# Kernel optimization log

Hardware: AMD Instinct MI355X
Metric: run time of the kernel (lower is better)

The kernel has to match this reference:

```python
import jax, jax.numpy as jnp
import numpy as np

D_MODEL = 1024
NHEAD = 16
EPS = 1e-5


def layer_norm(x, scale, bias):
    mu = jnp.mean(x, axis=-1, keepdims=True)
    var = jnp.var(x, axis=-1, keepdims=True)
    return (x - mu) * jax.lax.rsqrt(var + EPS) * scale + bias


def setup_inputs() -> dict:
    key = jax.random.key(0)
    ks = jax.random.split(key, 8)
    B, S, D = 4, 2048, D_MODEL
    s = 1.0 / np.sqrt(D)
    return {
        "x": jax.random.normal(ks[0], (B, S, D), dtype=jnp.float32),
        "Wq": jax.random.normal(ks[1], (D, D), dtype=jnp.float32) * s,
        "Wk": jax.random.normal(ks[2], (D, D), dtype=jnp.float32) * s,
        "Wv": jax.random.normal(ks[3], (D, D), dtype=jnp.float32) * s,
        "W1": jax.random.normal(ks[4], (D, D), dtype=jnp.float32) * s,
        "b1": jnp.zeros((D,), dtype=jnp.float32),
        "W2": jax.random.normal(ks[5], (D, D), dtype=jnp.float32) * s,
        "b2": jnp.zeros((D,), dtype=jnp.float32),
        "ln1_scale": jnp.ones((D,), dtype=jnp.float32),
        "ln1_bias": jnp.zeros((D,), dtype=jnp.float32),
        "ln2_scale": jnp.ones((D,), dtype=jnp.float32),
        "ln2_bias": jnp.zeros((D,), dtype=jnp.float32),
    }


def reference(x, Wq, Wk, Wv, W1, b1, W2, b2, ln1_scale, ln1_bias, ln2_scale, ln2_bias):
    B, S, D = x.shape
    H = NHEAD
    dh = D // H
    x = layer_norm(x, ln1_scale, ln1_bias)
    # torch Linear: y = x @ W.T (no bias for q/k/v)
    q = jnp.einsum('bsd,ed->bse', x, Wq).reshape(B, S, H, dh).transpose(0, 2, 1, 3)
    k = jnp.einsum('bsd,ed->bse', x, Wk).reshape(B, S, H, dh).transpose(0, 2, 1, 3)
    v = jnp.einsum('bsd,ed->bse', x, Wv).reshape(B, S, H, dh).transpose(0, 2, 1, 3)
    # NOTE: original module applies NO 1/sqrt(dh) scaling — kept faithful.
    scores = jnp.einsum('bhqd,bhkd->bhqk', q, k)
    attn = jax.nn.softmax(scores, axis=-1)  # dropout is identity in eval
    att = jnp.einsum('bhqk,bhkd->bhqd', attn, v)
    att = att.transpose(0, 2, 1, 3).reshape(B, S, D)
    xt = layer_norm(x + att, ln2_scale, ln2_bias)
    h = jax.nn.relu(jnp.einsum('bsd,ed->bse', xt, W1) + b1)
    ffn = jnp.einsum('bsd,ed->bse', h, W2) + b2
    return xt + ffn
```

## Files before the change

kernel.cpp:

```cpp
#include <hip/hip_runtime.h>
#include <stdint.h>

typedef unsigned short u16;
typedef __attribute__((ext_vector_type(4))) float f32x4;
typedef _Float16 h16;
typedef __attribute__((ext_vector_type(8))) _Float16 f16x8;
typedef __attribute__((ext_vector_type(4))) _Float16 h16x4;
typedef __attribute__((ext_vector_type(2))) __fp16 fp16v2;

#define DMODEL 1024
#define SEQ    2048
#define BATCH  4
#define NHEAD  16
#define DH     64
#define NTOK   (BATCH*SEQ)
#define BH     (BATCH*NHEAD)
#define EPS    1e-5f
#define LOG2E  1.44269504f

__device__ __forceinline__ void gload_lds16(const void* g, void* l){
  __builtin_amdgcn_global_load_lds((__attribute__((address_space(1))) unsigned int*)g,
                                   (__attribute__((address_space(3))) unsigned int*)l,
                                   16, 0, 0);
}

__device__ __forceinline__ float fastexp2(float x){
#if __has_builtin(__builtin_amdgcn_exp2f)
  return __builtin_amdgcn_exp2f(x);
#else
  return exp2f(x);
#endif
}

__device__ __forceinline__ int swzkey(int row){ return (row&7) ^ ((row>>3)&7); }

__global__ __launch_bounds__(256) void prep_weights(const float* __restrict__ Wq,
                                                    const float* __restrict__ Wk,
                                                    const float* __restrict__ Wv,
                                                    const float* __restrict__ W1,
                                                    const float* __restrict__ W2,
                                                    h16* __restrict__ wqkv,
                                                    h16* __restrict__ w1h,
                                                    h16* __restrict__ w2h){
  const int nW = DMODEL*DMODEL;
  int r = blockIdx.x >> 10;
  int i = ((blockIdx.x & 1023)*256 + threadIdx.x)*4;
  const float* src = (r==0) ? Wq : (r==1) ? Wk : (r==2) ? Wv : (r==3) ? W1 : W2;
  h16* dst = (r==0) ? wqkv : (r==1) ? (wqkv+nW) : (r==2) ? (wqkv+2*nW) : (r==3) ? w1h : w2h;
  float4 v = *reinterpret_cast<const float4*>(src + i);
  h16x4 o; o[0]=(h16)v.x; o[1]=(h16)v.y; o[2]=(h16)v.z; o[3]=(h16)v.w;
  *reinterpret_cast<h16x4*>(dst + i) = o;
}

__global__ __launch_bounds__(256) void ln_kernel(const float* __restrict__ in0,
                                                 const float* __restrict__ sc,
                                                 const float* __restrict__ bi,
                                                 float* __restrict__ of32,
                                                 h16* __restrict__ oh16){
  int row = blockIdx.x*4 + (threadIdx.x>>6);
  int l = threadIdx.x & 63;
  size_t rbase = (size_t)row*DMODEL;
  float v[16];
  #pragma unroll
  for (int q=0;q<4;++q){
    float4 t = *reinterpret_cast<const float4*>(in0 + rbase + q*256 + l*4);
    v[q*4]=t.x; v[q*4+1]=t.y; v[q*4+2]=t.z; v[q*4+3]=t.w;
  }
  float s=0.f, ss=0.f;
  #pragma unroll
  for (int j=0;j<16;++j){ s += v[j]; ss += v[j]*v[j]; }
  #pragma unroll
  for (int m=1;m<64;m<<=1){ s += __shfl_xor(s,m); ss += __shfl_xor(ss,m); }
  float mu  = s * (1.0f/DMODEL);
  float var = fmaxf(ss * (1.0f/DMODEL) - mu*mu, 0.0f);
  float r = rsqrtf(var + EPS);
  #pragma unroll
  for (int q=0;q<4;++q){
    float4 g = *reinterpret_cast<const float4*>(sc + q*256 + l*4);
    float4 b = *reinterpret_cast<const float4*>(bi + q*256 + l*4);
    float o0 = (v[q*4  ]-mu)*r*g.x + b.x;
    float o1 = (v[q*4+1]-mu)*r*g.y + b.y;
    float o2 = (v[q*4+2]-mu)*r*g.z + b.z;
    float o3 = (v[q*4+3]-mu)*r*g.w + b.w;
    size_t off = rbase + q*256 + l*4;
    if (of32){
      float4 ov; ov.x=o0; ov.y=o1; ov.z=o2; ov.w=o3;
      *reinterpret_cast<float4*>(of32 + off) = ov;
    }
    if (oh16){
      h16x4 oh; oh[0]=(h16)o0; oh[1]=(h16)o1; oh[2]=(h16)o2; oh[3]=(h16)o3;
      *reinterpret_cast<h16x4*>(oh16 + off) = oh;
    }
  }
}

__global__ __launch_bounds__(256) void gemm_qkv(const h16* __restrict__ xn,
                                                const h16* __restrict__ wqkv,
                                                h16* __restrict__ qT,
                                                h16* __restrict__ kR,
                                                h16* __restrict__ vT){
  const int K = DMODEL;
  __shared__ h16 As[2][128*64], Bs[2][128*64];
  int id = blockIdx.x;
  int xcd = id & 7, j = id >> 3;
  int bm = xcd*8 + j/24;
  int bn = j - (j/24)*24;
  int t = threadIdx.x, l = t&63, w = t>>6;
  int wr = w>>1, wc = w&1;
  const h16* Bsrc = wqkv + (size_t)bn*128*K;

  f32x4 acc[4][4];
  #pragma unroll
  for (int m=0;m<4;++m)
    #pragma unroll
    for (int n=0;n<4;++n)
      #pragma unroll
      for (int i=0;i<4;++i) acc[m][n][i] = 0.0f;

  #define QSTAGE(bb, k0)                                                          \
    { _Pragma("unroll")                                                           \
      for (int i_=0;i_<4;++i_){                                                   \
        int slot = i_*256 + t;                                                    \
        int row = slot>>3, pc = slot&7;                                           \
        int lc = pc ^ swzkey(row);                                                \
        gload_lds16(xn + (size_t)(bm*128 + row)*K + (k0) + lc*8, &As[bb][slot*8]);\
        gload_lds16(Bsrc + (size_t)row*K + (k0) + lc*8, &Bs[bb][slot*8]);         \
      } }

  const int nk = K/64;
  QSTAGE(0, 0);
  int cur = 0;
  for (int kt=0; kt<nk; ++kt){
    __syncthreads();
    if (kt+1 < nk) QSTAGE(cur^1, (kt+1)*64);
    #pragma unroll
    for (int ks=0; ks<2; ++ks){
      f16x8 af[4], bf[4];
      #pragma unroll
      for (int m=0;m<4;++m){
        int row = wr*64 + m*16 + (l&15);
        int cp = (ks*4 + (l>>4)) ^ swzkey(row);
        af[m] = *reinterpret_cast<const f16x8*>(&As[cur][row*64 + cp*8]);
      }
      #pragma unroll
      for (int n=0;n<4;++n){
        int row = wc*64 + n*16 + (l&15);
        int cp = (ks*4 + (l>>4)) ^ swzkey(row);
        bf[n] = *reinterpret_cast<const f16x8*>(&Bs[cur][row*64 + cp*8]);
      }
      __builtin_amdgcn_s_setprio(1);
      #pragma unroll
      for (int m=0;m<4;++m)
        #pragma unroll
        for (int n=0;n<4;++n)
          acc[m][n] = __builtin_amdgcn_mfma_f32_16x16x32_f16(af[m], bf[n], acc[m][n], 0,0,0);
      __builtin_amdgcn_s_setprio(0);
    }
    cur ^= 1;
  }

  const bool isK = (bn >= 8 && bn < 16);
  const bool isQ = (bn < 8);
  #pragma unroll
  for (int m=0;m<4;++m){
    int row0 = bm*128 + wr*64 + m*16 + ((l>>4)<<2);
    int b = row0 >> 11, s0 = row0 & 2047;
    #pragma unroll
    for (int n=0;n<4;++n){
      int col = bn*128 + wc*64 + n*16 + (l&15);
      int dg = col & 1023;
      int hh = dg >> 6, dh = dg & 63;
      if (isK){
        #pragma unroll
        for (int i=0;i<4;++i)
          kR[((size_t)(b*NHEAD + hh)*SEQ + s0 + i)*DH + dh] = (h16)acc[m][n][i];
      } else {
        h16x4 ov;
        #pragma unroll
        for (int i=0;i<4;++i){
          float vv = acc[m][n][i];
          if (isQ) vv *= LOG2E;
          ov[i] = (h16)vv;
        }
        int s0p = isQ ? s0 : ((s0 & ~31) + (((s0>>2)&3)<<3) + (((s0>>4)&1)<<2));
        h16* dst = (isQ ? qT : vT) + ((size_t)(b*NHEAD + hh)*DH + dh)*SEQ + s0p;
        *reinterpret_cast<h16x4*>(dst) = ov;
      }
    }
  }
}

template<bool RELU, bool RES, bool OUTF32>
__global__ __launch_bounds__(256) void gemm_ffn(const h16* __restrict__ A,
                                                const h16* __restrict__ W,
                                                const float* __restrict__ bias,
                                                const float* __restrict__ resid,
                                                void* __restrict__ outp,
                                                int M, int N, int K){
  __shared__ h16 As[2][128*64];
  __shared__ h16 Bs[2][128*64];
  int id = blockIdx.x;
  int xcd = id & 7, j = id >> 3;
  int nbn = N >> 7;
  int bm = xcd*((M>>7)>>3) + j/nbn;
  int bn = j - (j/nbn)*nbn;
  int t = threadIdx.x, l = t&63, w = t>>6;
  int wr = w>>1, wc = w&1;
  f32x4 acc[4][4];
  #pragma unroll
  for (int m=0;m<4;++m)
    #pragma unroll
    for (int n=0;n<4;++n)
      #pragma unroll
      for (int i=0;i<4;++i) acc[m][n][i] = 0.0f;

  #define FSTAGE(bb, k0)                                                          \
    { _Pragma("unroll")                                                           \
      for (int i_=0;i_<4;++i_){                                                   \
        int slot = i_*256 + t;                                                    \
        int row = slot>>3, pc = slot&7;                                           \
        int lc = pc ^ swzkey(row);                                                \
        gload_lds16(A + (size_t)(bm*128 + row)*K + (k0) + lc*8, &As[bb][slot*8]); \
        gload_lds16(W + (size_t)(bn*128 + row)*K + (k0) + lc*8, &Bs[bb][slot*8]); \
      } }

  const int nk = K/64;
  FSTAGE(0, 0);
  int cur = 0;
  for (int kt=0; kt<nk; ++kt){
    __syncthreads();
    if (kt+1 < nk) FSTAGE(cur^1, (kt+1)*64);
    #pragma unroll
    for (int ks=0; ks<2; ++ks){
      f16x8 af[4], bf[4];
      #pragma unroll
      for (int m=0;m<4;++m){
        int row = wr*64 + m*16 + (l&15);
        int cp = (ks*4 + (l>>4)) ^ swzkey(row);
        af[m] = *reinterpret_cast<const f16x8*>(&As[cur][row*64 + cp*8]);
      }
      #pragma unroll
      for (int n=0;n<4;++n){
        int row = wc*64 + n*16 + (l&15);
        int cp = (ks*4 + (l>>4)) ^ swzkey(row);
        bf[n] = *reinterpret_cast<const f16x8*>(&Bs[cur][row*64 + cp*8]);
      }
      __builtin_amdgcn_s_setprio(1);
      #pragma unroll
      for (int m=0;m<4;++m)
        #pragma unroll
        for (int n=0;n<4;++n)
          acc[m][n] = __builtin_amdgcn_mfma_f32_16x16x32_f16(af[m], bf[n], acc[m][n], 0,0,0);
      __builtin_amdgcn_s_setprio(0);
    }
    cur ^= 1;
  }

  #pragma unroll
  for (int m=0;m<4;++m){
    int row0 = bm*128 + wr*64 + m*16 + ((l>>4)<<2);
    #pragma unroll
    for (int n=0;n<4;++n){
      int col = bn*128 + wc*64 + n*16 + (l&15);
      float bv = bias[col];
      #pragma unroll
      for (int i=0;i<4;++i){
        float vv = acc[m][n][i] + bv;
        if (RELU) vv = fmaxf(vv, 0.0f);
        size_t off = (size_t)(row0+i)*N + col;
        if (RES) vv += resid[off];
        if (OUTF32) ((float*)outp)[off] = vv;
        else        ((h16*)outp)[off] = (h16)vv;
      }
    }
  }
}

#define QBLK 256
#define KBLK 64
#define RESC_THR_L2 11.5415603f
#define NROWS (BH*8*256)

__global__ __launch_bounds__(512, 2) void attn_split(const h16* __restrict__ qT,
                                                     const h16* __restrict__ kR,
                                                     const h16* __restrict__ vT,
                                                     h16* __restrict__ outP0,
                                                     h16* __restrict__ outP1,
                                                     float2* __restrict__ lm){
  int id = blockIdx.x;
  int bh   = (id & 7) + ((id >> 7) << 3);
  int qb   = (id >> 3) & 7;
  int half = (id >> 6) & 1;
  int t = threadIdx.x, l = t&63, w = t>>6;
  int g = l>>4;

  const size_t hbase = (size_t)bh * SEQ * DH;
  const h16* khb = kR + hbase + (size_t)half*(SEQ/2)*DH;
  const h16* qtb = qT + hbase;
  const h16* vtb = vT + hbase + half*(SEQ/2);
  int q0 = qb*QBLK + w*32;

  f16x8 qf[2][2];
  #pragma unroll
  for (int qs=0;qs<2;++qs)
    #pragma unroll
    for (int kc=0;kc<2;++kc)
      #pragma unroll
      for (int j=0;j<8;++j)
        qf[qs][kc][j] = qtb[(size_t)(kc*32 + g*8 + j)*SEQ + q0 + qs*16 + (l&15)];

  __shared__ h16 Kh2[2][KBLK*64];
  __shared__ h16 Vt2[2][KBLK*64];

  int offs[8];
  #pragma unroll
  for (int kc=0;kc<2;++kc)
    #pragma unroll
    for (int st=0;st<4;++st){
      int rr = st*16 + (l&15);
      offs[kc*4+st] = rr*128 + (((kc*4 + g) ^ swzkey(rr))<<4);
    }

  int srow = t>>3, spc = t&7;
  int slc = spc ^ swzkey(srow);
  const h16* ksrc = khb + (size_t)srow*DH + slc*8;
  const h16* vsrc = vtb + (size_t)srow*SEQ + slc*8;

  f32x4 o[2][4];
  #pragma unroll
  for (int qs=0;qs<2;++qs)
    #pragma unroll
    for (int dt=0;dt<4;++dt)
      #pragma unroll
      for (int i=0;i<4;++i) o[qs][dt][i] = 0.0f;
  f32x4 lacc[2];
  #pragma unroll
  for (int qs=0;qs<2;++qs)
    #pragma unroll
    for (int i=0;i<4;++i) lacc[qs][i] = 0.0f;
  float m_run[2] = {-3.0e38f, -3.0e38f};

  f16x8 onesA;
  #pragma unroll
  for (int j=0;j<8;++j) onesA[j] = (h16)1.0f;

  #define STAGE(bb)                                  \
    { gload_lds16(ksrc, &Kh2[bb][t*8]);              \
      gload_lds16(vsrc, &Vt2[bb][t*8]);              \
      ksrc += KBLK*DH; vsrc += KBLK; }

  STAGE(0);
  int cur = 0;
  const int NT = SEQ/2/KBLK;
  for (int kt=0; kt<NT; ++kt){
    __syncthreads();
    if (kt+1 < NT) STAGE(cur^1);

    char* KhB = (char*)&Kh2[cur][0];
    char* VtB = (char*)&Vt2[cur][0];

    f32x4 sc[2][4];
    #pragma unroll
    for (int qs=0;qs<2;++qs)
      #pragma unroll
      for (int st=0;st<4;++st)
        #pragma unroll
        for (int i=0;i<4;++i) sc[qs][st][i] = 0.0f;

    #pragma unroll
    for (int kc=0;kc<2;++kc)
      #pragma unroll
      for (int st=0;st<4;++st){
        f16x8 kf = *reinterpret_cast<const f16x8*>(KhB + offs[kc*4+st]);
        __builtin_amdgcn_s_setprio(1);
        sc[0][st] = __builtin_amdgcn_mfma_f32_16x16x32_f16(kf, qf[0][kc], sc[0][st], 0,0,0);
        sc[1][st] = __builtin_amdgcn_mfma_f32_16x16x32_f16(kf, qf[1][kc], sc[1][st], 0,0,0);
        __builtin_amdgcn_s_setprio(0);
      }

    float lmax[2];
    #pragma unroll
    for (int qs=0;qs<2;++qs){
      const float* s = (const float*)&sc[qs][0];
      float m0 = fmaxf(s[0], s[1]);
      #pragma unroll
      for (int j=2;j<16;j+=2) m0 = fmaxf(fmaxf(m0, s[j]), s[j+1]);
      lmax[qs] = m0;
    }
    bool defer = (__all((lmax[0] <= m_run[0] + RESC_THR_L2) &&
                        (lmax[1] <= m_run[1] + RESC_THR_L2)) != 0);
    if (!defer){
      #pragma unroll
      for (int qs=0;qs<2;++qs){
        float m0 = lmax[qs];
        m0 = fmaxf(m0, __shfl_xor(m0, 16));
        m0 = fmaxf(m0, __shfl_xor(m0, 32));
        float mn = fmaxf(m_run[qs], m0);
        float scl = fastexp2(m_run[qs] - mn);
        m_run[qs] = mn;
        #pragma unroll
        for (int dt=0;dt<4;++dt)
          #pragma unroll
          for (int i=0;i<4;++i) o[qs][dt][i] *= scl;
        #pragma unroll
        for (int i=0;i<4;++i) lacc[qs][i] *= scl;
      }
    }

    union { unsigned u[4]; f16x8 v; } pfu[2][2];
    #pragma unroll
    for (int qs=0;qs<2;++qs){
      float mn = m_run[qs];
      const float* s = (const float*)&sc[qs][0];
      #pragma unroll
      for (int kc=0;kc<2;++kc)
        #pragma unroll
        for (int j=0;j<4;++j){
          float p0 = fastexp2(s[kc*8+2*j]   - mn);
          float p1 = fastexp2(s[kc*8+2*j+1] - mn);
          union { fp16v2 v2; unsigned u; } c;
          c.v2 = __builtin_amdgcn_cvt_pkrtz(p0, p1);
          pfu[qs][kc].u[j] = c.u;
        }
    }

    #pragma unroll
    for (int kc=0;kc<2;++kc){
      __builtin_amdgcn_s_setprio(1);
      lacc[0] = __builtin_amdgcn_mfma_f32_16x16x32_f16(onesA, pfu[0][kc].v, lacc[0], 0,0,0);
      lacc[1] = __builtin_amdgcn_mfma_f32_16x16x32_f16(onesA, pfu[1][kc].v, lacc[1], 0,0,0);
      __builtin_amdgcn_s_setprio(0);
      #pragma unroll
      for (int dt=0;dt<4;++dt){
        f16x8 vf = *reinterpret_cast<const f16x8*>(VtB + offs[kc*4+dt]);
        __builtin_amdgcn_s_setprio(1);
        o[0][dt] = __builtin_amdgcn_mfma_f32_16x16x32_f16(vf, pfu[0][kc].v, o[0][dt], 0,0,0);
        o[1][dt] = __builtin_amdgcn_mfma_f32_16x16x32_f16(vf, pfu[1][kc].v, o[1][dt], 0,0,0);
        __builtin_amdgcn_s_setprio(0);
      }
    }
    cur ^= 1;
  }

  h16* outP = half ? outP1 : outP0;
  int rowbase = (bh*8 + qb)*256 + w*32;
  #pragma unroll
  for (int qs=0;qs<2;++qs){
    float lt = lacc[qs][0];
    float inv = 1.0f / lt;
    int row = rowbase + qs*16 + (l&15);
    #pragma unroll
    for (int dt=0;dt<4;++dt){
      h16x4 ov;
      #pragma unroll
      for (int i=0;i<4;++i) ov[i] = (h16)(o[qs][dt][i] * inv);
      *reinterpret_cast<h16x4*>(outP + (size_t)row*64 + dt*16 + (g<<2)) = ov;
    }
    if (l < 16)
      lm[half*NROWS + row] = make_float2(m_run[qs], lt);
  }
}

__global__ __launch_bounds__(256) void ln2_combine(const float* __restrict__ xn,
                                                   const h16* __restrict__ p0,
                                                   const h16* __restrict__ p1,
                                                   const float2* __restrict__ lm,
                                                   const float* __restrict__ sc,
                                                   const float* __restrict__ bi,
                                                   float* __restrict__ of32,
                                                   h16* __restrict__ oh16){
  int token = blockIdx.x*4 + (threadIdx.x>>6);
  int l = threadIdx.x & 63;
  int b = token >> 11, qb = (token >> 8) & 7, r = token & 255;
  int hh = l >> 2;
  int rowg = ((b*NHEAD + hh)*8 + qb)*256 + r;
  float2 A = lm[rowg];
  float2 B = lm[NROWS + rowg];
  float ms = fmaxf(A.x, B.x);
  float w0 = A.y * fastexp2(A.x - ms);
  float w1 = B.y * fastexp2(B.x - ms);
  float inv = 1.0f / (w0 + w1);
  w0 *= inv; w1 *= inv;

  const f16x8* q0 = reinterpret_cast<const f16x8*>(p0 + (size_t)rowg*64 + (l&3)*16);
  const f16x8* q1 = reinterpret_cast<const f16x8*>(p1 + (size_t)rowg*64 + (l&3)*16);
  size_t base = (size_t)token*DMODEL + l*16;
  float v[16];
  #pragma unroll
  for (int c=0;c<2;++c){
    f16x8 a = q0[c], bb = q1[c];
    #pragma unroll
    for (int j=0;j<8;++j)
      v[c*8+j] = (float)a[j]*w0 + (float)bb[j]*w1;
  }
  #pragma unroll
  for (int q=0;q<4;++q){
    float4 t = *reinterpret_cast<const float4*>(xn + base + q*4);
    v[q*4] += t.x; v[q*4+1] += t.y; v[q*4+2] += t.z; v[q*4+3] += t.w;
  }

  float s=0.f, ss=0.f;
  #pragma unroll
  for (int j=0;j<16;++j){ s += v[j]; ss += v[j]*v[j]; }
  #pragma unroll
  for (int m=1;m<64;m<<=1){ s += __shfl_xor(s,m); ss += __shfl_xor(ss,m); }
  float mu  = s * (1.0f/DMODEL);
  float var = fmaxf(ss * (1.0f/DMODEL) - mu*mu, 0.0f);
  float rr = rsqrtf(var + EPS);
  #pragma unroll
  for (int q=0;q<4;++q){
    float4 g = *reinterpret_cast<const float4*>(sc + l*16 + q*4);
    float4 bb = *reinterpret_cast<const float4*>(bi + l*16 + q*4);
    float o0 = (v[q*4  ]-mu)*rr*g.x + bb.x;
    float o1 = (v[q*4+1]-mu)*rr*g.y + bb.y;
    float o2 = (v[q*4+2]-mu)*rr*g.z + bb.z;
    float o3 = (v[q*4+3]-mu)*rr*g.w + bb.w;
    float4 ov; ov.x=o0; ov.y=o1; ov.z=o2; ov.w=o3;
    *reinterpret_cast<float4*>(of32 + base + q*4) = ov;
    h16x4 oh; oh[0]=(h16)o0; oh[1]=(h16)o1; oh[2]=(h16)o2; oh[3]=(h16)o3;
    *reinterpret_cast<h16x4*>(oh16 + base + q*4) = oh;
  }
}

extern "C" void kernel_launch(void* const* d_in, const int* in_sizes, int n_in,
                              void* d_out, int out_size, void* d_ws, size_t ws_size,
                              hipStream_t stream){
  (void)in_sizes; (void)n_in; (void)out_size; (void)ws_size;
  const float* x    = (const float*)d_in[0];
  const float* Wq   = (const float*)d_in[1];
  const float* Wk   = (const float*)d_in[2];
  const float* Wv   = (const float*)d_in[3];
  const float* W1   = (const float*)d_in[4];
  const float* b1   = (const float*)d_in[5];
  const float* W2   = (const float*)d_in[6];
  const float* b2   = (const float*)d_in[7];
  const float* ln1s = (const float*)d_in[8];
  const float* ln1b = (const float*)d_in[9];
  const float* ln2s = (const float*)d_in[10];
  const float* ln2b = (const float*)d_in[11];

  char* ws = (char*)d_ws;
  float* xn_f32  = (float*)ws;  ws += (size_t)NTOK*DMODEL*4;
  h16* part0     = (h16*)ws;    ws += (size_t)NTOK*DMODEL*2;
  h16* part1     = (h16*)ws;    ws += (size_t)NTOK*DMODEL*2;
  float* xt_f32  = (float*)ws;  ws += (size_t)NTOK*DMODEL*4;
  h16* xn_h      = (h16*)ws;    ws += (size_t)NTOK*DMODEL*2;
  h16* qT_h      = (h16*)ws;    ws += (size_t)NTOK*DMODEL*2;
  h16* k_h       = (h16*)ws;    ws += (size_t)NTOK*DMODEL*2;
  h16* vT_h      = (h16*)ws;    ws += (size_t)NTOK*DMODEL*2;
  h16* xt_h      = (h16*)ws;    ws += (size_t)NTOK*DMODEL*2;
  h16* h_h       = (h16*)ws;    ws += (size_t)NTOK*DMODEL*2;
  h16* wqkv_h    = (h16*)ws;    ws += (size_t)3*DMODEL*DMODEL*2;
  h16* w1h       = (h16*)ws;    ws += (size_t)DMODEL*DMODEL*2;
  h16* w2h       = (h16*)ws;    ws += (size_t)DMODEL*DMODEL*2;
  float2* lm     = (float2*)ws; ws += (size_t)2*NROWS*8;

  prep_weights<<<5120, 256, 0, stream>>>(Wq, Wk, Wv, W1, W2, wqkv_h, w1h, w2h);

  ln_kernel<<<NTOK/4, 256, 0, stream>>>(x, ln1s, ln1b, xn_f32, xn_h);

  gemm_qkv<<<3*DMODEL/128 * (NTOK/128), 256, 0, stream>>>(
      xn_h, wqkv_h, qT_h, k_h, vT_h);

  attn_split<<<BH*(SEQ/QBLK)*2, 512, 0, stream>>>(qT_h, k_h, vT_h, part0, part1, lm);

  ln2_combine<<<NTOK/4, 256, 0, stream>>>(xn_f32, part0, part1, lm,
                                          ln2s, ln2b, xt_f32, xt_h);

  gemm_ffn<true,false,false><<<(DMODEL/128) * (NTOK/128), 256, 0, stream>>>(
      xt_h, w1h, b1, nullptr, h_h, NTOK, DMODEL, DMODEL);

  gemm_ffn<false,true,true><<<(DMODEL/128) * (NTOK/128), 256, 0, stream>>>(
      h_h, w2h, b2, xt_f32, d_out, NTOK, DMODEL, DMODEL);
}
```

Measured before the change: 270.9 us.

## Drop fp32 activation copies, fuse weight prep with LN1, reorder GEMM block mapping

```diff
diff --git a/kernel.cpp b/kernel.cpp
--- a/kernel.cpp
+++ b/kernel.cpp
@@ -34,37 +34,39 @@
 
 __device__ __forceinline__ int swzkey(int row){ return (row&7) ^ ((row>>3)&7); }
 
-__global__ __launch_bounds__(256) void prep_weights(const float* __restrict__ Wq,
-                                                    const float* __restrict__ Wk,
-                                                    const float* __restrict__ Wv,
-                                                    const float* __restrict__ W1,
-                                                    const float* __restrict__ W2,
-                                                    h16* __restrict__ wqkv,
-                                                    h16* __restrict__ w1h,
-                                                    h16* __restrict__ w2h){
-  const int nW = DMODEL*DMODEL;
-  int r = blockIdx.x >> 10;
-  int i = ((blockIdx.x & 1023)*256 + threadIdx.x)*4;
-  const float* src = (r==0) ? Wq : (r==1) ? Wk : (r==2) ? Wv : (r==3) ? W1 : W2;
-  h16* dst = (r==0) ? wqkv : (r==1) ? (wqkv+nW) : (r==2) ? (wqkv+2*nW) : (r==3) ? w1h : w2h;
-  float4 v = *reinterpret_cast<const float4*>(src + i);
-  h16x4 o; o[0]=(h16)v.x; o[1]=(h16)v.y; o[2]=(h16)v.z; o[3]=(h16)v.w;
-  *reinterpret_cast<h16x4*>(dst + i) = o;
-}
-
-__global__ __launch_bounds__(256) void ln_kernel(const float* __restrict__ in0,
-                                                 const float* __restrict__ sc,
-                                                 const float* __restrict__ bi,
-                                                 float* __restrict__ of32,
-                                                 h16* __restrict__ oh16){
-  int row = blockIdx.x*4 + (threadIdx.x>>6);
-  int l = threadIdx.x & 63;
+__global__ __launch_bounds__(256) void prep_ln(const float* __restrict__ Wq,
+                                               const float* __restrict__ Wk,
+                                               const float* __restrict__ Wv,
+                                               const float* __restrict__ W1,
+                                               const float* __restrict__ W2,
+                                               h16* __restrict__ wqkv,
+                                               h16* __restrict__ w1h,
+                                               h16* __restrict__ w2h,
+                                               const float* __restrict__ x,
+                                               const float* __restrict__ sc,
+                                               const float* __restrict__ bi,
+                                               h16* __restrict__ xn_h){
+  int id = blockIdx.x;
+  int t = threadIdx.x;
+  if (id < 5120){
+    const int nW = DMODEL*DMODEL;
+    int r = id >> 10;
+    int i = ((id & 1023)*256 + t)*4;
+    const float* src = (r==0) ? Wq : (r==1) ? Wk : (r==2) ? Wv : (r==3) ? W1 : W2;
+    h16* dst = (r==0) ? wqkv : (r==1) ? (wqkv+nW) : (r==2) ? (wqkv+2*nW) : (r==3) ? w1h : w2h;
+    float4 v = *reinterpret_cast<const float4*>(src + i);
+    h16x4 o; o[0]=(h16)v.x; o[1]=(h16)v.y; o[2]=(h16)v.z; o[3]=(h16)v.w;
+    *reinterpret_cast<h16x4*>(dst + i) = o;
+    return;
+  }
+  int row = (id - 5120)*4 + (t>>6);
+  int l = t & 63;
   size_t rbase = (size_t)row*DMODEL;
   float v[16];
   #pragma unroll
   for (int q=0;q<4;++q){
-    float4 t = *reinterpret_cast<const float4*>(in0 + rbase + q*256 + l*4);
-    v[q*4]=t.x; v[q*4+1]=t.y; v[q*4+2]=t.z; v[q*4+3]=t.w;
+    float4 tt = *reinterpret_cast<const float4*>(x + rbase + q*256 + l*4);
+    v[q*4]=tt.x; v[q*4+1]=tt.y; v[q*4+2]=tt.z; v[q*4+3]=tt.w;
   }
   float s=0.f, ss=0.f;
   #pragma unroll
@@ -78,19 +80,12 @@
   for (int q=0;q<4;++q){
     float4 g = *reinterpret_cast<const float4*>(sc + q*256 + l*4);
     float4 b = *reinterpret_cast<const float4*>(bi + q*256 + l*4);
-    float o0 = (v[q*4  ]-mu)*r*g.x + b.x;
-    float o1 = (v[q*4+1]-mu)*r*g.y + b.y;
-    float o2 = (v[q*4+2]-mu)*r*g.z + b.z;
-    float o3 = (v[q*4+3]-mu)*r*g.w + b.w;
-    size_t off = rbase + q*256 + l*4;
-    if (of32){
-      float4 ov; ov.x=o0; ov.y=o1; ov.z=o2; ov.w=o3;
-      *reinterpret_cast<float4*>(of32 + off) = ov;
-    }
-    if (oh16){
-      h16x4 oh; oh[0]=(h16)o0; oh[1]=(h16)o1; oh[2]=(h16)o2; oh[3]=(h16)o3;
-      *reinterpret_cast<h16x4*>(oh16 + off) = oh;
-    }
+    h16x4 oh;
+    oh[0] = (h16)((v[q*4  ]-mu)*r*g.x + b.x);
+    oh[1] = (h16)((v[q*4+1]-mu)*r*g.y + b.y);
+    oh[2] = (h16)((v[q*4+2]-mu)*r*g.z + b.z);
+    oh[3] = (h16)((v[q*4+3]-mu)*r*g.w + b.w);
+    *reinterpret_cast<h16x4*>(xn_h + rbase + q*256 + l*4) = oh;
   }
 }
 
@@ -103,8 +98,8 @@
   __shared__ h16 As[2][128*64], Bs[2][128*64];
   int id = blockIdx.x;
   int xcd = id & 7, j = id >> 3;
-  int bm = xcd*8 + j/24;
-  int bn = j - (j/24)*24;
+  int bn = j >> 3;
+  int bm = xcd*8 + (j & 7);
   int t = threadIdx.x, l = t&63, w = t>>6;
   int wr = w>>1, wc = w&1;
   const h16* Bsrc = wqkv + (size_t)bn*128*K;
@@ -194,16 +189,16 @@
 __global__ __launch_bounds__(256) void gemm_ffn(const h16* __restrict__ A,
                                                 const h16* __restrict__ W,
                                                 const float* __restrict__ bias,
-                                                const float* __restrict__ resid,
+                                                const h16* __restrict__ resid,
                                                 void* __restrict__ outp,
                                                 int M, int N, int K){
   __shared__ h16 As[2][128*64];
   __shared__ h16 Bs[2][128*64];
   int id = blockIdx.x;
   int xcd = id & 7, j = id >> 3;
-  int nbn = N >> 7;
-  int bm = xcd*((M>>7)>>3) + j/nbn;
-  int bn = j - (j/nbn)*nbn;
+  int spb = (M>>7)>>3;
+  int bn = j / spb;
+  int bm = xcd*spb + (j - bn*spb);
   int t = threadIdx.x, l = t&63, w = t>>6;
   int wr = w>>1, wc = w&1;
   f32x4 acc[4][4];
@@ -268,7 +263,7 @@
         float vv = acc[m][n][i] + bv;
         if (RELU) vv = fmaxf(vv, 0.0f);
         size_t off = (size_t)(row0+i)*N + col;
-        if (RES) vv += resid[off];
+        if (RES) vv += (float)resid[off];
         if (OUTF32) ((float*)outp)[off] = vv;
         else        ((h16*)outp)[off] = (h16)vv;
       }
@@ -461,13 +456,12 @@
   }
 }
 
-__global__ __launch_bounds__(256) void ln2_combine(const float* __restrict__ xn,
+__global__ __launch_bounds__(256) void ln2_combine(const h16* __restrict__ xn,
                                                    const h16* __restrict__ p0,
                                                    const h16* __restrict__ p1,
                                                    const float2* __restrict__ lm,
                                                    const float* __restrict__ sc,
                                                    const float* __restrict__ bi,
-                                                   float* __restrict__ of32,
                                                    h16* __restrict__ oh16){
   int token = blockIdx.x*4 + (threadIdx.x>>6);
   int l = threadIdx.x & 63;
@@ -494,9 +488,11 @@
       v[c*8+j] = (float)a[j]*w0 + (float)bb[j]*w1;
   }
   #pragma unroll
-  for (int q=0;q<4;++q){
-    float4 t = *reinterpret_cast<const float4*>(xn + base + q*4);
-    v[q*4] += t.x; v[q*4+1] += t.y; v[q*4+2] += t.z; v[q*4+3] += t.w;
+  for (int c=0;c<2;++c){
+    f16x8 xv = *reinterpret_cast<const f16x8*>(xn + base + c*8);
+    #pragma unroll
+    for (int j=0;j<8;++j)
+      v[c*8+j] += (float)xv[j];
   }
 
   float s=0.f, ss=0.f;
@@ -511,13 +507,11 @@
   for (int q=0;q<4;++q){
     float4 g = *reinterpret_cast<const float4*>(sc + l*16 + q*4);
     float4 bb = *reinterpret_cast<const float4*>(bi + l*16 + q*4);
-    float o0 = (v[q*4  ]-mu)*rr*g.x + bb.x;
-    float o1 = (v[q*4+1]-mu)*rr*g.y + bb.y;
-    float o2 = (v[q*4+2]-mu)*rr*g.z + bb.z;
-    float o3 = (v[q*4+3]-mu)*rr*g.w + bb.w;
-    float4 ov; ov.x=o0; ov.y=o1; ov.z=o2; ov.w=o3;
-    *reinterpret_cast<float4*>(of32 + base + q*4) = ov;
-    h16x4 oh; oh[0]=(h16)o0; oh[1]=(h16)o1; oh[2]=(h16)o2; oh[3]=(h16)o3;
+    h16x4 oh;
+    oh[0] = (h16)((v[q*4  ]-mu)*rr*g.x + bb.x);
+    oh[1] = (h16)((v[q*4+1]-mu)*rr*g.y + bb.y);
+    oh[2] = (h16)((v[q*4+2]-mu)*rr*g.z + bb.z);
+    oh[3] = (h16)((v[q*4+3]-mu)*rr*g.w + bb.w);
     *reinterpret_cast<h16x4*>(oh16 + base + q*4) = oh;
   }
 }
@@ -540,10 +534,8 @@
   const float* ln2b = (const float*)d_in[11];
 
   char* ws = (char*)d_ws;
-  float* xn_f32  = (float*)ws;  ws += (size_t)NTOK*DMODEL*4;
   h16* part0     = (h16*)ws;    ws += (size_t)NTOK*DMODEL*2;
   h16* part1     = (h16*)ws;    ws += (size_t)NTOK*DMODEL*2;
-  float* xt_f32  = (float*)ws;  ws += (size_t)NTOK*DMODEL*4;
   h16* xn_h      = (h16*)ws;    ws += (size_t)NTOK*DMODEL*2;
   h16* qT_h      = (h16*)ws;    ws += (size_t)NTOK*DMODEL*2;
   h16* k_h       = (h16*)ws;    ws += (size_t)NTOK*DMODEL*2;
@@ -555,21 +547,20 @@
   h16* w2h       = (h16*)ws;    ws += (size_t)DMODEL*DMODEL*2;
   float2* lm     = (float2*)ws; ws += (size_t)2*NROWS*8;
 
-  prep_weights<<<5120, 256, 0, stream>>>(Wq, Wk, Wv, W1, W2, wqkv_h, w1h, w2h);
-
-  ln_kernel<<<NTOK/4, 256, 0, stream>>>(x, ln1s, ln1b, xn_f32, xn_h);
+  prep_ln<<<5120 + NTOK/4, 256, 0, stream>>>(Wq, Wk, Wv, W1, W2, wqkv_h, w1h, w2h,
+                                             x, ln1s, ln1b, xn_h);
 
   gemm_qkv<<<3*DMODEL/128 * (NTOK/128), 256, 0, stream>>>(
       xn_h, wqkv_h, qT_h, k_h, vT_h);
 
   attn_split<<<BH*(SEQ/QBLK)*2, 512, 0, stream>>>(qT_h, k_h, vT_h, part0, part1, lm);
 
-  ln2_combine<<<NTOK/4, 256, 0, stream>>>(xn_f32, part0, part1, lm,
-                                          ln2s, ln2b, xt_f32, xt_h);
+  ln2_combine<<<NTOK/4, 256, 0, stream>>>(xn_h, part0, part1, lm,
+                                          ln2s, ln2b, xt_h);
 
   gemm_ffn<true,false,false><<<(DMODEL/128) * (NTOK/128), 256, 0, stream>>>(
       xt_h, w1h, b1, nullptr, h_h, NTOK, DMODEL, DMODEL);
 
   gemm_ffn<false,true,true><<<(DMODEL/128) * (NTOK/128), 256, 0, stream>>>(
-      h_h, w2h, b2, xt_f32, d_out, NTOK, DMODEL, DMODEL);
-}
+      h_h, w2h, b2, xt_h, d_out, NTOK, DMODEL, DMODEL);
+}
```

Measured after the change: 250.2 us (median of 2 runs). -7.7%, faster.
